# Kernel tuning notes

Measured on AMD Instinct MI355X. Metric: run time of the kernel, lower is better.

Reference implementation:

```python
import jax, jax.numpy as jnp
import numpy as np

N = 50000
E_RAND = 800000
F_IN = 128
H = 4          # num_heads
D_HID = 32     # hidden per-head dim
D_OUT = 32     # output per-head dim
NEG_SLOPE_ATTN = 0.2   # DGL GATConv attention leaky_relu
NEG_SLOPE_ACT = 0.01   # F.leaky_relu default activation


def setup_inputs() -> dict:
    key = jax.random.key(0)
    ks = jax.random.split(key, 12)
    x = jax.random.normal(ks[0], (N, F_IN), dtype=jnp.float32)
    src_r = jax.random.randint(ks[1], (E_RAND,), 0, N, dtype=jnp.int32)
    dst_r = jax.random.randint(ks[2], (E_RAND,), 0, N, dtype=jnp.int32)
    loop = jnp.arange(N, dtype=jnp.int32)
    src = jnp.concatenate([src_r, loop])  # add_self_loop
    dst = jnp.concatenate([dst_r, loop])
    sc1 = 1.0 / np.sqrt(F_IN)
    sc2 = 1.0 / np.sqrt(H * D_HID)
    W1 = jax.random.normal(ks[3], (F_IN, H * D_HID), dtype=jnp.float32) * sc1
    al1 = jax.random.normal(ks[4], (H, D_HID), dtype=jnp.float32) * sc1
    ar1 = jax.random.normal(ks[5], (H, D_HID), dtype=jnp.float32) * sc1
    b1 = jnp.zeros((H * D_HID,), dtype=jnp.float32)
    W2 = jax.random.normal(ks[6], (H * D_HID, H * D_OUT), dtype=jnp.float32) * sc2
    al2 = jax.random.normal(ks[7], (H, D_OUT), dtype=jnp.float32) * sc2
    ar2 = jax.random.normal(ks[8], (H, D_OUT), dtype=jnp.float32) * sc2
    b2 = jnp.zeros((H * D_OUT,), dtype=jnp.float32)
    return {"x": x, "src": src, "dst": dst,
            "W1": W1, "al1": al1, "ar1": ar1, "b1": b1,
            "W2": W2, "al2": al2, "ar2": ar2, "b2": b2}


def gat_conv(x, src, dst, W, al, ar, b, act_slope):
    n = x.shape[0]
    h, d = al.shape
    feat = (x @ W).reshape(n, h, d)                 # [N,H,D]
    el = jnp.einsum('nhd,hd->nh', feat, al)         # [N,H]
    er = jnp.einsum('nhd,hd->nh', feat, ar)
    # edge attention score on edge u->v: leaky_relu(el[u] + er[v])
    e = jax.nn.leaky_relu(el[src] + er[dst], NEG_SLOPE_ATTN)  # [E,H]
    # edge softmax over incoming edges of each dst node (self-loops guarantee >=1 edge)
    m = jax.ops.segment_max(e, dst, num_segments=n)           # [N,H]
    ex = jnp.exp(e - m[dst])
    s = jax.ops.segment_sum(ex, dst, num_segments=n)
    a = ex / s[dst]                                           # [E,H]
    # attention-weighted scatter-sum of source features
    out = jax.ops.segment_sum(a[:, :, None] * feat[src], dst, num_segments=n)  # [N,H,D]
    out = out + b.reshape(h, d)
    if act_slope is not None:
        out = jax.nn.leaky_relu(out, act_slope)
    return out.reshape(n, h * d)                    # flatten(1)


def reference(x, src, dst, W1, al1, ar1, b1, W2, al2, ar2, b2):
    h = gat_conv(x, src, dst, W1, al1, ar1, b1, NEG_SLOPE_ACT)
    out = gat_conv(h, src, dst, W2, al2, ar2, b2, None)  # last layer: no activation
    return out
```

## Files before the change

kernel.cpp:

```cpp
#include <hip/hip_runtime.h>
#include <hip/hip_bf16.h>
#include <hip/hip_fp16.h>

#define HEADS 4
#define DHEAD 32
#define FDIM 128
#define BCAP 64

__global__ __launch_bounds__(256) void k_gemm(
    const float* __restrict__ X, const float* __restrict__ W,
    const float* __restrict__ al, const float* __restrict__ ar,
    __half* __restrict__ feat, float* __restrict__ el, float* __restrict__ er, int n,
    const int* __restrict__ esrc, const int* __restrict__ edst,
    int* __restrict__ deg, int* __restrict__ bucket, int E) {
    __shared__ float Wl[FDIM * DHEAD];
    int head = blockIdx.y;

    if (E > 0 && head == 0) {
        int nb = gridDim.x;
        int echunk = (E + nb - 1) / nb;
        int e0 = blockIdx.x * echunk;
        int e1 = e0 + echunk; if (e1 > E) e1 = E;
        for (int base = e0 + threadIdx.x; base < e1; base += 256 * 8) {
            int d[8], s[8];
#pragma unroll
            for (int j = 0; j < 8; j++) {
                int idx = base + j * 256;
                if (idx < e1) { d[j] = edst[idx]; s[j] = esrc[idx]; }
                else d[j] = -1;
            }
#pragma unroll
            for (int j = 0; j < 8; j++) {
                if (d[j] >= 0) {
                    int p = atomicAdd(&deg[d[j]], 1);
                    if (p < BCAP) bucket[((size_t)d[j] << 6) + p] = s[j];
                }
            }
        }
    }

    {
        float4* Wl4 = (float4*)Wl;
        for (int i = threadIdx.x; i < FDIM * DHEAD / 4; i += 256) {
            int k = i >> 3, j4 = i & 7;
            Wl4[i] = ((const float4*)(W + (size_t)k * FDIM + head * DHEAD))[j4];
        }
    }
    __syncthreads();

    int wave = threadIdx.x >> 6;
    int lane = threadIdx.x & 63;
    int row = blockIdx.x * 256 + wave * 64 + lane;
    bool valid = row < n;
    int cr = valid ? row : (n - 1);
    const float4* xp = (const float4*)(X + (size_t)cr * FDIM);

    float acc[32];
#pragma unroll
    for (int j = 0; j < 32; j++) acc[j] = 0.f;

    float4 a = xp[0];
    for (int k4 = 0; k4 < FDIM / 4; k4++) {
        float4 an = (k4 < FDIM / 4 - 1) ? xp[k4 + 1] : a;
#pragma unroll
        for (int kk = 0; kk < 4; kk++) {
            const float4* wr = (const float4*)(Wl + (k4 * 4 + kk) * DHEAD);
            float s = (&a.x)[kk];
#pragma unroll
            for (int j4 = 0; j4 < 8; j4++) {
                float4 wv = wr[j4];
                acc[j4 * 4 + 0] += s * wv.x;
                acc[j4 * 4 + 1] += s * wv.y;
                acc[j4 * 4 + 2] += s * wv.z;
                acc[j4 * 4 + 3] += s * wv.w;
            }
        }
        a = an;
    }

    float elv = 0.f, erv = 0.f;
#pragma unroll
    for (int j = 0; j < 32; j++) {
        elv += acc[j] * al[head * DHEAD + j];
        erv += acc[j] * ar[head * DHEAD + j];
    }
    if (valid) {
        el[(size_t)row * HEADS + head] = elv;
        er[(size_t)row * HEADS + head] = erv;
    }

    if (valid) {
        union { __half2 h2[16]; uint4 u4[4]; } pk;
#pragma unroll
        for (int m = 0; m < 16; m++)
            pk.h2[m] = __floats2half2_rn(acc[2 * m], acc[2 * m + 1]);
        uint4* dstp = (uint4*)(feat + (size_t)row * FDIM + head * DHEAD);
#pragma unroll
        for (int t = 0; t < 4; t++) dstp[t] = pk.u4[t];
    }
}

__global__ __launch_bounds__(256) void k_aggregate(
    const int* __restrict__ bucket, const int* __restrict__ deg,
    const __half2* __restrict__ feat2h, const float* __restrict__ el,
    const float* __restrict__ er, const float* __restrict__ b,
    float* __restrict__ out, int n, int apply_act) {
    int wave = threadIdx.x >> 6;
    int node = blockIdx.x * 4 + wave;
    if (node >= n) return;
    node = __builtin_amdgcn_readfirstlane(node);
    int lane = threadIdx.x & 63;
    int h = lane >> 4;

    float ern = er[(size_t)node * HEADS + h];
    int cnt = __builtin_amdgcn_readfirstlane(deg[node]);
    const int* bkt = bucket + ((size_t)node << 6);

    float ax = 0.f, ay = 0.f, sw = 0.f;
    int i = 0;

    for (; i + 8 <= cnt; i += 8) {
        int s[8];
#pragma unroll
        for (int j = 0; j < 8; j++) s[j] = bkt[i + j];
        float e[8];
#pragma unroll
        for (int j = 0; j < 8; j++) e[j] = el[(size_t)s[j] * HEADS + h];
        __half2 f[8];
#pragma unroll
        for (int j = 0; j < 8; j++) f[j] = feat2h[(size_t)s[j] * 64 + lane];
#pragma unroll
        for (int j = 0; j < 8; j++) {
            float ev = e[j] + ern;
            ev = ev > 0.f ? ev : 0.2f * ev;
            float w = __expf(ev);
            float2 fv = __half22float2(f[j]);
            sw += w; ax += w * fv.x; ay += w * fv.y;
        }
    }
    for (; i + 2 <= cnt; i += 2) {
        int s0 = bkt[i], s1 = bkt[i + 1];
        float e0 = el[(size_t)s0 * HEADS + h];
        float e1 = el[(size_t)s1 * HEADS + h];
        __half2 f0 = feat2h[(size_t)s0 * 64 + lane];
        __half2 f1 = feat2h[(size_t)s1 * 64 + lane];
        e0 += ern; e0 = e0 > 0.f ? e0 : 0.2f * e0;
        e1 += ern; e1 = e1 > 0.f ? e1 : 0.2f * e1;
        float w0 = __expf(e0), w1 = __expf(e1);
        float2 fv0 = __half22float2(f0), fv1 = __half22float2(f1);
        sw += w0 + w1;
        ax += w0 * fv0.x + w1 * fv1.x;
        ay += w0 * fv0.y + w1 * fv1.y;
    }
    if (i < cnt) {
        int s0 = bkt[i];
        float e0 = el[(size_t)s0 * HEADS + h] + ern;
        e0 = e0 > 0.f ? e0 : 0.2f * e0;
        float w0 = __expf(e0);
        float2 fv0 = __half22float2(feat2h[(size_t)s0 * 64 + lane]);
        sw += w0; ax += w0 * fv0.x; ay += w0 * fv0.y;
    }

    float inv = 1.0f / sw;
    float2 bv = ((const float2*)b)[lane];
    float ox = ax * inv + bv.x;
    float oy = ay * inv + bv.y;
    if (apply_act) {
        ox = ox > 0.f ? ox : 0.01f * ox;
        oy = oy > 0.f ? oy : 0.01f * oy;
    }
    float2 o; o.x = ox; o.y = oy;
    ((float2*)out)[(size_t)node * 64 + lane] = o;
}


extern "C" void kernel_launch(void* const* d_in, const int* in_sizes, int n_in,
                              void* d_out, int out_size, void* d_ws, size_t ws_size,
                              hipStream_t stream) {
    const float* x   = (const float*)d_in[0];
    const int*   src = (const int*)d_in[1];
    const int*   dst = (const int*)d_in[2];
    const float* W1  = (const float*)d_in[3];
    const float* al1 = (const float*)d_in[4];
    const float* ar1 = (const float*)d_in[5];
    const float* b1  = (const float*)d_in[6];
    const float* W2  = (const float*)d_in[7];
    const float* al2 = (const float*)d_in[8];
    const float* ar2 = (const float*)d_in[9];
    const float* b2  = (const float*)d_in[10];
    int N = in_sizes[0] / FDIM;
    int E = in_sizes[1];
    float* out = (float*)d_out;

    __half* featA = (__half*)d_ws;
    float* elb    = (float*)(featA + (size_t)N * FDIM);
    float* erb    = elb + (size_t)N * HEADS;
    int*   deg    = (int*)(erb + (size_t)N * HEADS);
    int*   bucket = deg + N;
    float* hbuf   = out;

    int gx = (N + 255) / 256;
    dim3 ggrid(gx, HEADS);

    hipMemsetAsync(deg, 0, (size_t)N * sizeof(int), stream);

    k_gemm<<<ggrid, 256, 0, stream>>>(x, W1, al1, ar1, featA, elb, erb, N,
                                      src, dst, deg, bucket, E);
    k_aggregate<<<(N + 3) / 4, 256, 0, stream>>>(bucket, deg, (const __half2*)featA,
                                                 elb, erb, b1, hbuf, N, 1);

    k_gemm<<<ggrid, 256, 0, stream>>>(hbuf, W2, al2, ar2, featA, elb, erb, N,
                                      nullptr, nullptr, nullptr, nullptr, 0);
    k_aggregate<<<(N + 3) / 4, 256, 0, stream>>>(bucket, deg, (const __half2*)featA,
                                                 elb, erb, b2, out, N, 0);
}
```

Before: 298.2 us.

## Stage X rows in LDS and read W via scalar loads per wave-head

The GEMM kernel now processes 64 rows per block, with each of the 4 waves computing one head for the same 64 rows. The X tile is staged into padded shared memory so all four heads reuse it. W is read straight from global memory with a wave-uniform address, so it can go through scalar loads instead of an LDS copy. This removes the 4x redundant X reads across heads and the per-block W LDS fill, at the cost of 4x more blocks and edge-bucketing work now spread over every block.

```diff
diff --git a/kernel.cpp b/kernel.cpp
--- a/kernel.cpp
+++ b/kernel.cpp
@@ -6,6 +6,8 @@
 #define DHEAD 32
 #define FDIM 128
 #define BCAP 64
+#define RPB 64
+#define XPAD (FDIM/4 + 1)
 
 __global__ __launch_bounds__(256) void k_gemm(
     const float* __restrict__ X, const float* __restrict__ W,
@@ -13,10 +15,9 @@
     __half* __restrict__ feat, float* __restrict__ el, float* __restrict__ er, int n,
     const int* __restrict__ esrc, const int* __restrict__ edst,
     int* __restrict__ deg, int* __restrict__ bucket, int E) {
-    __shared__ float Wl[FDIM * DHEAD];
-    int head = blockIdx.y;
-
-    if (E > 0 && head == 0) {
+    __shared__ float Xs[RPB * 4 * XPAD];
+
+    if (E > 0) {
         int nb = gridDim.x;
         int echunk = (E + nb - 1) / nb;
         int e0 = blockIdx.x * echunk;
@@ -39,32 +40,37 @@
         }
     }
 
+    int r0 = blockIdx.x * RPB;
+    int rowsLeft = n - r0; if (rowsLeft > RPB) rowsLeft = RPB;
     {
-        float4* Wl4 = (float4*)Wl;
-        for (int i = threadIdx.x; i < FDIM * DHEAD / 4; i += 256) {
-            int k = i >> 3, j4 = i & 7;
-            Wl4[i] = ((const float4*)(W + (size_t)k * FDIM + head * DHEAD))[j4];
+        float4* xsw = (float4*)Xs;
+        const float4* Xg = (const float4*)(X + (size_t)r0 * FDIM);
+        for (int i = threadIdx.x; i < RPB * (FDIM / 4); i += 256) {
+            int row = i >> 5, c4 = i & 31;
+            int sr = row < rowsLeft ? row : 0;
+            xsw[row * XPAD + c4] = Xg[(size_t)sr * (FDIM / 4) + c4];
         }
     }
     __syncthreads();
 
-    int wave = threadIdx.x >> 6;
+    int head = __builtin_amdgcn_readfirstlane(threadIdx.x >> 6);
     int lane = threadIdx.x & 63;
-    int row = blockIdx.x * 256 + wave * 64 + lane;
+    int row = r0 + lane;
     bool valid = row < n;
-    int cr = valid ? row : (n - 1);
-    const float4* xp = (const float4*)(X + (size_t)cr * FDIM);
+
+    const float4* xs4 = (const float4*)Xs + (size_t)lane * XPAD;
+    const float* wb = W + head * DHEAD;
 
     float acc[32];
 #pragma unroll
     for (int j = 0; j < 32; j++) acc[j] = 0.f;
 
-    float4 a = xp[0];
+#pragma unroll 4
     for (int k4 = 0; k4 < FDIM / 4; k4++) {
-        float4 an = (k4 < FDIM / 4 - 1) ? xp[k4 + 1] : a;
+        float4 a = xs4[k4];
 #pragma unroll
         for (int kk = 0; kk < 4; kk++) {
-            const float4* wr = (const float4*)(Wl + (k4 * 4 + kk) * DHEAD);
+            const float4* wr = (const float4*)(wb + (size_t)(k4 * 4 + kk) * FDIM);
             float s = (&a.x)[kk];
 #pragma unroll
             for (int j4 = 0; j4 < 8; j4++) {
@@ -75,7 +81,6 @@
                 acc[j4 * 4 + 3] += s * wv.w;
             }
         }
-        a = an;
     }
 
     float elv = 0.f, erv = 0.f;
@@ -199,18 +204,17 @@
     int*   bucket = deg + N;
     float* hbuf   = out;
 
-    int gx = (N + 255) / 256;
-    dim3 ggrid(gx, HEADS);
+    int gblocks = (N + RPB - 1) / RPB;
 
     hipMemsetAsync(deg, 0, (size_t)N * sizeof(int), stream);
 
-    k_gemm<<<ggrid, 256, 0, stream>>>(x, W1, al1, ar1, featA, elb, erb, N,
-                                      src, dst, deg, bucket, E);
+    k_gemm<<<gblocks, 256, 0, stream>>>(x, W1, al1, ar1, featA, elb, erb, N,
+                                        src, dst, deg, bucket, E);
     k_aggregate<<<(N + 3) / 4, 256, 0, stream>>>(bucket, deg, (const __half2*)featA,
                                                  elb, erb, b1, hbuf, N, 1);
 
-    k_gemm<<<ggrid, 256, 0, stream>>>(hbuf, W2, al2, ar2, featA, elb, erb, N,
-                                      nullptr, nullptr, nullptr, nullptr, 0);
+    k_gemm<<<gblocks, 256, 0, stream>>>(hbuf, W2, al2, ar2, featA, elb, erb, N,
+                                        nullptr, nullptr, nullptr, nullptr, 0);
     k_aggregate<<<(N + 3) / 4, 256, 0, stream>>>(bucket, deg, (const __half2*)featA,
                                                  elb, erb, b2, out, N, 0);
 }
```

New measurement: 264.9 us. 11.2% less time.
